# Kernel tuning notes

Hardware: AMD Instinct MI355X
Metric: run time of the kernel (lower is better)

The kernel has to match this reference:

```python
import jax, jax.numpy as jnp
import numpy as np

LMAX1, LMAX2 = 2, 2
LMAX_OUT = LMAX1 + LMAX2  # FullTensorProduct output lmax
BATCH, MUL = 50000, 512


def _make_cg(l1max, l2max, l3max):
    """Dense CG-like tensor with the true SO(3) selection-rule block sparsity.

    Shape [(l1max+1)^2, (l2max+1)^2, (l3max+1)^2]; blocks outside
    |l1-l2| <= l3 <= l1+l2 are exactly zero, matching so3.clebsch_gordan's
    sparsity pattern (values here are random stand-ins; the einsum math is
    identical for any coefficient values).
    """
    d1, d2, d3 = (l1max + 1) ** 2, (l2max + 1) ** 2, (l3max + 1) ** 2
    cg = np.zeros((d1, d2, d3), dtype=np.float32)
    rng = np.random.default_rng(0)
    for l1 in range(l1max + 1):
        for l2 in range(l2max + 1):
            for l3 in range(abs(l1 - l2), min(l1 + l2, l3max) + 1):
                s1, s2, s3 = l1 * l1, l2 * l2, l3 * l3
                blk = rng.standard_normal((2 * l1 + 1, 2 * l2 + 1, 2 * l3 + 1))
                cg[s1:s1 + 2 * l1 + 1, s2:s2 + 2 * l2 + 1, s3:s3 + 2 * l3 + 1] = (
                    blk / np.sqrt(2.0 * l3 + 1.0)).astype(np.float32)
    return jnp.asarray(cg)


def setup_inputs() -> dict:
    key = jax.random.key(0)
    k1, k2 = jax.random.split(key)
    d1 = (LMAX1 + 1) ** 2  # 9
    d2 = (LMAX2 + 1) ** 2  # 9
    x1 = jax.random.normal(k1, (BATCH, d1, MUL), dtype=jnp.float32)
    x2 = jax.random.normal(k2, (BATCH, d2, MUL), dtype=jnp.float32)
    cg = _make_cg(LMAX1, LMAX2, LMAX_OUT)  # [9, 9, 25]
    return {"x1": x1, "x2": x2, "cg": cg}


def reference(x1, x2, cg):
    # TensorProduct.forward, non-pseudotensor path, channel_dim == 'f':
    # torch.einsum('...lf, ...mf, lmn -> ...nf', x1, x2, cg)
    return jnp.einsum('blf,bmf,lmn->bnf', x1, x2, cg)
```

## Files before the change

kernel.cpp:

```cpp
#include <hip/hip_runtime.h>


#define BATCH 50000
#define MUL   512
#define D3    25
#define FCHUNK 256
#define ROWB  208
#define RPB   10

typedef __bf16 bf16x8 __attribute__((ext_vector_type(8)));
typedef float  f32x4  __attribute__((ext_vector_type(4)));

__global__ void __launch_bounds__(256) tp_kernel(
    const float* __restrict__ x1,
    const float* __restrict__ x2,
    const float* __restrict__ cg,
    float* __restrict__ out) {

    extern __shared__ char smem[];

    const int bg    = blockIdx.x >> 1;
    const int chunk = blockIdx.x & 1;
    const int tid   = threadIdx.x;
    const int lane  = tid & 63;
    const int wv    = tid >> 6;
    const int b0    = bg * RPB;

    bf16x8 afrag[2][3];
    #pragma unroll
    for (int mt = 0; mt < 2; ++mt) {
        const int n = 16 * mt + (lane & 15);
        #pragma unroll
        for (int ks = 0; ks < 3; ++ks) {
            #pragma unroll
            for (int j = 0; j < 8; ++j) {
                const int k = 32 * ks + 8 * (lane >> 4) + j;
                float w = (k < 81 && n < D3) ? cg[k * D3 + n] : 0.0f;
                afrag[mt][ks][j] = (__bf16)w;
            }
        }
    }

    const int fl = chunk * FCHUNK + tid;
    const float* x1p = x1 + (size_t)b0 * (9 * MUL) + fl;
    const float* x2p = x2 + (size_t)b0 * (9 * MUL) + fl;
    const int fg = chunk * FCHUNK + wv * 64 + (lane & 15);
    float* op = out + (size_t)b0 * (D3 * MUL) + fg;

    float a[9], c[9];
    #pragma unroll
    for (int l = 0; l < 9; ++l) a[l] = x1p[l * MUL];
    #pragma unroll
    for (int m = 0; m < 9; ++m) c[m] = x2p[m * MUL];

    uint4* row = reinterpret_cast<uint4*>(smem + tid * ROWB);
    const char* bbase0 = smem + (size_t)(wv * 64 + (lane & 15)) * ROWB
                              + (lane >> 4) * 16;

    for (int r = 0; r < RPB; ++r) {
        #pragma unroll
        for (int ch = 0; ch < 12; ++ch) {
            bf16x8 v;
            #pragma unroll
            for (int j = 0; j < 8; ++j) {
                const int k = ch * 8 + j;
                const float p = (k < 81) ? a[k / 9] * c[k % 9] : 0.0f;
                v[j] = (__bf16)p;
            }
            row[ch] = __builtin_bit_cast(uint4, v);
        }

        x1p += 9 * MUL;
        x2p += 9 * MUL;
        if (r != RPB - 1) {
            #pragma unroll
            for (int l = 0; l < 9; ++l) a[l] = x1p[l * MUL];
            #pragma unroll
            for (int m = 0; m < 9; ++m) c[m] = x2p[m * MUL];
        }

        f32x4 acc[2][4];
        #pragma unroll
        for (int mt = 0; mt < 2; ++mt)
            #pragma unroll
            for (int ft = 0; ft < 4; ++ft)
                acc[mt][ft] = (f32x4){0.f, 0.f, 0.f, 0.f};

        #pragma unroll
        for (int ft = 0; ft < 4; ++ft) {
            const char* bb = bbase0 + ft * 16 * ROWB;
            #pragma unroll
            for (int ks = 0; ks < 3; ++ks) {
                bf16x8 bfrag = *reinterpret_cast<const bf16x8*>(bb + ks * 64);
                acc[0][ft] = __builtin_amdgcn_mfma_f32_16x16x32_bf16(
                    afrag[0][ks], bfrag, acc[0][ft], 0, 0, 0);
                acc[1][ft] = __builtin_amdgcn_mfma_f32_16x16x32_bf16(
                    afrag[1][ks], bfrag, acc[1][ft], 0, 0, 0);
            }
        }

        #pragma unroll
        for (int mt = 0; mt < 2; ++mt) {
            #pragma unroll
            for (int rr = 0; rr < 4; ++rr) {
                const int n = 16 * mt + (lane >> 4) * 4 + rr;
                if (n < D3) {
                    #pragma unroll
                    for (int ft = 0; ft < 4; ++ft)
                        __builtin_nontemporal_store(
                            acc[mt][ft][rr], op + (size_t)n * MUL + ft * 16);
                }
            }
        }
        op += D3 * MUL;
    }
}

extern "C" void kernel_launch(void* const* d_in, const int* in_sizes, int n_in,
                              void* d_out, int out_size, void* d_ws, size_t ws_size,
                              hipStream_t stream) {
    const float* x1 = (const float*)d_in[0];
    const float* x2 = (const float*)d_in[1];
    const float* cg = (const float*)d_in[2];
    float* out = (float*)d_out;

    dim3 grid((BATCH / RPB) * 2);
    dim3 block(256);
    tp_kernel<<<grid, block, FCHUNK * ROWB, stream>>>(x1, x2, cg, out);
}
```

Measured before the change: 858.1 us.

## Process full feature width per block and stage output through LDS for vector stores

Each block now covers all 512 features, with every thread loading two features as float2, instead of splitting the work into two 256-feature chunks. The MFMA tile count per wave doubles. Accumulators are transposed through a per-wave LDS scratch area so each row can be written with 16-byte nontemporal stores, replacing scalar strided stores. In exchange, the block's LDS footprint doubles to about 106 KB, which limits residency to roughly one block per CU and may weaken latency hiding in this memory-bound kernel.

```diff
diff --git a/kernel.cpp b/kernel.cpp
--- a/kernel.cpp
+++ b/kernel.cpp
@@ -4,9 +4,10 @@
 #define BATCH 50000
 #define MUL   512
 #define D3    25
-#define FCHUNK 256
 #define ROWB  208
+#define TROW  132
 #define RPB   10
+#define SMEM_BYTES (512 * ROWB)
 
 typedef __bf16 bf16x8 __attribute__((ext_vector_type(8)));
 typedef float  f32x4  __attribute__((ext_vector_type(4)));
@@ -19,12 +20,22 @@
 
     extern __shared__ char smem[];
 
-    const int bg    = blockIdx.x >> 1;
-    const int chunk = blockIdx.x & 1;
-    const int tid   = threadIdx.x;
-    const int lane  = tid & 63;
-    const int wv    = tid >> 6;
-    const int b0    = bg * RPB;
+    const int bg   = blockIdx.x;
+    const int tid  = threadIdx.x;
+    const int lane = tid & 63;
+    const int wv   = tid >> 6;
+    const int b0   = bg * RPB;
+
+    const float2* x1v = reinterpret_cast<const float2*>(
+                            x1 + (size_t)b0 * (9 * MUL)) + tid;
+    const float2* x2v = reinterpret_cast<const float2*>(
+                            x2 + (size_t)b0 * (9 * MUL)) + tid;
+
+    float2 a[9], c[9];
+    #pragma unroll
+    for (int l = 0; l < 9; ++l) a[l] = x1v[l * 256];
+    #pragma unroll
+    for (int m = 0; m < 9; ++m) c[m] = x2v[m * 256];
 
     bf16x8 afrag[2][3];
     #pragma unroll
@@ -41,53 +52,51 @@
         }
     }
 
-    const int fl = chunk * FCHUNK + tid;
-    const float* x1p = x1 + (size_t)b0 * (9 * MUL) + fl;
-    const float* x2p = x2 + (size_t)b0 * (9 * MUL) + fl;
-    const int fg = chunk * FCHUNK + wv * 64 + (lane & 15);
-    float* op = out + (size_t)b0 * (D3 * MUL) + fg;
+    float* op = out + (size_t)b0 * (D3 * MUL) + wv * 128;
 
-    float a[9], c[9];
-    #pragma unroll
-    for (int l = 0; l < 9; ++l) a[l] = x1p[l * MUL];
-    #pragma unroll
-    for (int m = 0; m < 9; ++m) c[m] = x2p[m * MUL];
-
-    uint4* row = reinterpret_cast<uint4*>(smem + tid * ROWB);
-    const char* bbase0 = smem + (size_t)(wv * 64 + (lane & 15)) * ROWB
+    uint4* row0 = reinterpret_cast<uint4*>(smem + (size_t)tid * (2 * ROWB));
+    uint4* row1 = reinterpret_cast<uint4*>(smem + (size_t)tid * (2 * ROWB) + ROWB);
+    const char* bbase0 = smem + (size_t)(wv * 128 + (lane & 15)) * ROWB
                               + (lane >> 4) * 16;
+    float* twave = reinterpret_cast<float*>(smem + (size_t)wv * 128 * ROWB);
 
     for (int r = 0; r < RPB; ++r) {
         #pragma unroll
         for (int ch = 0; ch < 12; ++ch) {
-            bf16x8 v;
+            bf16x8 v0, v1;
             #pragma unroll
             for (int j = 0; j < 8; ++j) {
                 const int k = ch * 8 + j;
-                const float p = (k < 81) ? a[k / 9] * c[k % 9] : 0.0f;
-                v[j] = (__bf16)p;
+                float plo = 0.0f, phi = 0.0f;
+                if (k < 81) {
+                    plo = a[k / 9].x * c[k % 9].x;
+                    phi = a[k / 9].y * c[k % 9].y;
+                }
+                v0[j] = (__bf16)plo;
+                v1[j] = (__bf16)phi;
             }
-            row[ch] = __builtin_bit_cast(uint4, v);
+            row0[ch] = __builtin_bit_cast(uint4, v0);
+            row1[ch] = __builtin_bit_cast(uint4, v1);
         }
 
-        x1p += 9 * MUL;
-        x2p += 9 * MUL;
+        x1v += 9 * 256;
+        x2v += 9 * 256;
         if (r != RPB - 1) {
             #pragma unroll
-            for (int l = 0; l < 9; ++l) a[l] = x1p[l * MUL];
+            for (int l = 0; l < 9; ++l) a[l] = x1v[l * 256];
             #pragma unroll
-            for (int m = 0; m < 9; ++m) c[m] = x2p[m * MUL];
+            for (int m = 0; m < 9; ++m) c[m] = x2v[m * 256];
         }
 
-        f32x4 acc[2][4];
+        f32x4 acc[2][8];
         #pragma unroll
         for (int mt = 0; mt < 2; ++mt)
             #pragma unroll
-            for (int ft = 0; ft < 4; ++ft)
+            for (int ft = 0; ft < 8; ++ft)
                 acc[mt][ft] = (f32x4){0.f, 0.f, 0.f, 0.f};
 
         #pragma unroll
-        for (int ft = 0; ft < 4; ++ft) {
+        for (int ft = 0; ft < 8; ++ft) {
             const char* bb = bbase0 + ft * 16 * ROWB;
             #pragma unroll
             for (int ks = 0; ks < 3; ++ks) {
@@ -106,10 +115,23 @@
                 const int n = 16 * mt + (lane >> 4) * 4 + rr;
                 if (n < D3) {
                     #pragma unroll
-                    for (int ft = 0; ft < 4; ++ft)
-                        __builtin_nontemporal_store(
-                            acc[mt][ft][rr], op + (size_t)n * MUL + ft * 16);
+                    for (int ft = 0; ft < 8; ++ft)
+                        twave[n * TROW + ft * 16 + (lane & 15)]
+                            = acc[mt][ft][rr];
                 }
+            }
+        }
+
+        #pragma unroll
+        for (int idx = 0; idx < 13; ++idx) {
+            const int p = idx * 64 + lane;
+            if (p < D3 * 32) {
+                const int n = p >> 5;
+                const int q = p & 31;
+                const f32x4 v = *reinterpret_cast<const f32x4*>(
+                    twave + n * TROW + q * 4);
+                __builtin_nontemporal_store(
+                    v, reinterpret_cast<f32x4*>(op + (size_t)n * MUL + q * 4));
             }
         }
         op += D3 * MUL;
@@ -124,7 +146,10 @@
     const float* cg = (const float*)d_in[2];
     float* out = (float*)d_out;
 
-    dim3 grid((BATCH / RPB) * 2);
+    hipFuncSetAttribute(reinterpret_cast<const void*>(tp_kernel),
+                        hipFuncAttributeMaxDynamicSharedMemorySize, SMEM_BYTES);
+
+    dim3 grid(BATCH / RPB);
     dim3 block(256);
-    tp_kernel<<<grid, block, FCHUNK * ROWB, stream>>>(x1, x2, cg, out);
+    tp_kernel<<<grid, block, SMEM_BYTES, stream>>>(x1, x2, cg, out);
 }
```

Result: no change. 843.5 us (-1.7%).
